# Kernel tuning notes

Measured on AMD Instinct MI355X. Metric: run time of the kernel, lower is better.

## Reference

```python
import jax, jax.numpy as jnp
import numpy as np

QLEN, MLEN, BSZ = 1024, 1024, 2
KLEN = QLEN + MLEN           # 2048, also rlen
D_MODEL, N_HEAD, D_HEAD = 1024, 16, 64
SCALE = 1.0 / (D_HEAD ** 0.5)
LN_EPS = 1e-5


def _rel_shift(x):
    # x: (qlen, klen, bsz, n_head). Torch-XL rel_shift via pad/reshape trick.
    q, k, b, n = x.shape
    zero_pad = jnp.zeros((q, 1, b, n), dtype=x.dtype)
    x_padded = jnp.concatenate([zero_pad, x], axis=1)   # (q, k+1, b, n)
    x_padded = x_padded.reshape(k + 1, q, b, n)[1:]      # drop first row
    return x_padded.reshape(q, k, b, n)


def _layer_norm(x, g, b):
    mu = jnp.mean(x, axis=-1, keepdims=True)
    var = jnp.mean(jnp.square(x - mu), axis=-1, keepdims=True)
    return (x - mu) * jax.lax.rsqrt(var + LN_EPS) * g + b


def setup_inputs() -> dict:
    key = jax.random.key(0)
    ks = jax.random.split(key, 9)
    w = jax.random.normal(ks[0], (QLEN, BSZ, D_MODEL), dtype=jnp.float32)
    r = jax.random.normal(ks[1], (KLEN, D_MODEL), dtype=jnp.float32)
    mems = jax.random.normal(ks[2], (MLEN, BSZ, D_MODEL), dtype=jnp.float32)
    # Causal mask with memory: query i may attend to key j <= i + MLEN.
    i = jnp.arange(QLEN)[:, None]
    j = jnp.arange(KLEN)[None, :]
    attn_mask = (j > i + MLEN)[:, :, None]  # (qlen, klen, 1) bool, dim==3 branch
    init = 0.02
    qkv_w = jax.random.normal(ks[3], (3 * N_HEAD * D_HEAD, D_MODEL), dtype=jnp.float32) * init
    r_w = jax.random.normal(ks[4], (N_HEAD * D_HEAD, D_MODEL), dtype=jnp.float32) * init
    o_w = jax.random.normal(ks[5], (D_MODEL, N_HEAD * D_HEAD), dtype=jnp.float32) * init
    ln_g = jnp.ones((D_MODEL,), dtype=jnp.float32)
    ln_b = jnp.zeros((D_MODEL,), dtype=jnp.float32)
    r_w_bias = jax.random.uniform(ks[6], (N_HEAD, D_HEAD), minval=-0.1, maxval=0.1, dtype=jnp.float32)
    r_r_bias = jax.random.uniform(ks[7], (N_HEAD, D_HEAD), minval=-0.1, maxval=0.1, dtype=jnp.float32)
    return {"w": w, "r": r, "mems": mems, "attn_mask": attn_mask,
            "qkv_w": qkv_w, "r_w": r_w, "o_w": o_w,
            "ln_g": ln_g, "ln_b": ln_b,
            "r_w_bias": r_w_bias, "r_r_bias": r_r_bias}


def reference(w, r, mems, attn_mask, qkv_w, r_w, o_w, ln_g, ln_b, r_w_bias, r_r_bias):
    qlen, bsz = w.shape[0], w.shape[1]
    cat = jnp.concatenate([mems, w], axis=0)                 # (klen, b, d_model)
    w_heads = cat @ qkv_w.T                                  # (klen, b, 3*n*d)
    w_head_q, w_head_k, w_head_v = jnp.split(w_heads, 3, axis=-1)
    klen = w_head_k.shape[0]
    w_head_q = w_head_q[-qlen:].reshape(qlen, bsz, N_HEAD, D_HEAD)
    w_head_k = w_head_k.reshape(klen, bsz, N_HEAD, D_HEAD)
    w_head_v = w_head_v.reshape(klen, bsz, N_HEAD, D_HEAD)
    r_head_k = (r @ r_w.T).reshape(r.shape[0], N_HEAD, D_HEAD)  # (rlen, n, d)

    AC = jnp.einsum('ibnd,jbnd->ijbn', w_head_q + r_w_bias, w_head_k)
    BD = _rel_shift(jnp.einsum('ibnd,jnd->ijbn', w_head_q + r_r_bias, r_head_k))
    attn_score = (AC + BD) * SCALE                           # (q, k, b, n)
    attn_score = jnp.where(attn_mask[:, :, :, None], -jnp.inf, attn_score)
    attn_prob = jax.nn.softmax(attn_score, axis=1)           # softmax over keys

    attn_vec = jnp.einsum('ijbn,jbnd->ibnd', attn_prob, w_head_v)
    attn_vec = attn_vec.reshape(qlen, bsz, N_HEAD * D_HEAD)
    attn_out = attn_vec @ o_w.T                              # (q, b, d_model)
    # post-LN residual (pre_lnorm=False)
    return _layer_norm(w + attn_out, ln_g, ln_b)
```

## Files before the change

### kernel.cpp

```cpp
#include <hip/hip_runtime.h>
#include <hip/hip_bf16.h>

#define QLEN 1024
#define MLEN 1024
#define KLEN 2048
#define BSZ 2
#define DMODEL 1024
#define NHEAD 16
#define DHEAD 64
#define SCALE_F 0.125f

typedef unsigned int u32;
typedef unsigned short u16;
typedef __attribute__((ext_vector_type(8))) short short8;
typedef __attribute__((ext_vector_type(4))) float f32x4;

__device__ __forceinline__ u16 f2bf(float f) {
  __hip_bfloat16 h = __float2bfloat16(f);
  return *reinterpret_cast<u16*>(&h);
}
__device__ __forceinline__ float bf2f(u16 u) {
  union { u32 w; float f; } c; c.w = ((u32)u) << 16; return c.f;
}
__device__ __forceinline__ float wave_sum(float v) {
#pragma unroll
  for (int o = 32; o > 0; o >>= 1) v += __shfl_xor(v, o);
  return v;
}

__global__ void detect_kernel(const void* __restrict__ lng, u32* __restrict__ flag) {
  if (threadIdx.x == 0 && blockIdx.x == 0) {
    u32 w = *(const u32*)lng;
    *flag = (w == 0x3F800000u) ? 0u : 1u;
  }
}

__global__ void conv_params(const void* __restrict__ lng, const void* __restrict__ lnb,
                            const void* __restrict__ rwb, const void* __restrict__ rrb,
                            float* __restrict__ PARAMS) {
  int i = blockIdx.x * 256 + threadIdx.x;
  u32 w0 = *(const u32*)lng;
  int f = (w0 != 0x3F800000u);
  int seg = i >> 10, off = i & 1023;
  const void* s = seg == 0 ? lng : seg == 1 ? lnb : seg == 2 ? rwb : rrb;
  PARAMS[i] = f ? bf2f(((const u16*)s)[off]) : ((const float*)s)[off];
}

__global__ void sentinel_kernel(u32* out) { out[threadIdx.x] = 0x49742400u;  }


#define GEMM_PREAMBLE()                                                        \
  __shared__ __align__(16) char lds2[2][128 * 128];                            \
  char* lA = lds2[0];                                                          \
  char* lB = lds2[1];                                                          \
  const int tid = threadIdx.x;                                                 \
  const int w_ = tid >> 6, l_ = tid & 63, lo = l_ & 15, g = l_ >> 4;           \
  const int wr = (w_ >> 1) * 64, wc = (w_ & 1) * 64;                           \
  f32x4 acc[4][4];                                                             \
  _Pragma("unroll") for (int mi = 0; mi < 4; ++mi)                             \
  _Pragma("unroll") for (int ni = 0; ni < 4; ++ni)                             \
      acc[mi][ni] = (f32x4){0.f, 0.f, 0.f, 0.f};

#define GEMM_MFMA_BODY()                                                       \
  _Pragma("unroll") for (int ks = 0; ks < 2; ++ks) {                           \
    short8 af[4], bf[4];                                                       \
    _Pragma("unroll") for (int mi = 0; mi < 4; ++mi) {                         \
      int r = wr + mi * 16 + lo;                                               \
      int c = ks * 4 + g;                                                      \
      af[mi] = *reinterpret_cast<const short8*>(lA + r * 128 + ((c ^ (r & 7)) * 16)); \
    }                                                                          \
    _Pragma("unroll") for (int ni = 0; ni < 4; ++ni) {                         \
      int r = wc + ni * 16 + lo;                                               \
      int c = ks * 4 + g;                                                      \
      bf[ni] = *reinterpret_cast<const short8*>(lB + r * 128 + ((c ^ (r & 7)) * 16)); \
    }                                                                          \
    _Pragma("unroll") for (int mi = 0; mi < 4; ++mi)                           \
    _Pragma("unroll") for (int ni = 0; ni < 4; ++ni)                           \
        acc[mi][ni] = __builtin_amdgcn_mfma_f32_16x16x32_bf16(af[mi], bf[ni], acc[mi][ni], 0, 0, 0); \
  }

__device__ __forceinline__ uint4 cvt8f32(const float* p) {
  float4 a = *reinterpret_cast<const float4*>(p);
  float4 b4 = *reinterpret_cast<const float4*>(p + 4);
  union { u16 us[8]; uint4 v; } o;
  o.us[0] = f2bf(a.x); o.us[1] = f2bf(a.y); o.us[2] = f2bf(a.z); o.us[3] = f2bf(a.w);
  o.us[4] = f2bf(b4.x); o.us[5] = f2bf(b4.y); o.us[6] = f2bf(b4.z); o.us[7] = f2bf(b4.w);
  return o.v;
}

__global__ __launch_bounds__(256) void gemm_qkv(
    const void* __restrict__ mems_raw, const void* __restrict__ w_raw,
    const void* __restrict__ qkvw_raw,
    const void* __restrict__ r_raw, const void* __restrict__ rw_raw,
    const float* __restrict__ PARAMS,
    u16* __restrict__ QWb, u16* __restrict__ QRb,
    u16* __restrict__ Kb, u16* __restrict__ VTb, u16* __restrict__ RKnb,
    const u32* __restrict__ flag) {
  const int col0 = blockIdx.x * 128;
  const int row0 = blockIdx.y * 128;
  const int f = (int)*flag;
  GEMM_PREAMBLE();

  if (col0 < 1024 && row0 < 2048) {
    for (int k0 = 0; k0 < DMODEL; k0 += 64) {
      __syncthreads();
      if (f) {
#pragma unroll
        for (int it = 0; it < 4; ++it) {
          int id = it * 256 + tid;
          int r = id >> 3, c = id & 7;
          uint4 va = *reinterpret_cast<const uint4*>((const u16*)r_raw + (size_t)(row0 + r) * DMODEL + k0 + c * 8);
          uint4 vb = *reinterpret_cast<const uint4*>((const u16*)rw_raw + (size_t)(col0 + r) * DMODEL + k0 + c * 8);
          *reinterpret_cast<uint4*>(lA + r * 128 + ((c ^ (r & 7)) * 16)) = va;
          *reinterpret_cast<uint4*>(lB + r * 128 + ((c ^ (r & 7)) * 16)) = vb;
        }
      } else {
#pragma unroll
        for (int it = 0; it < 4; ++it) {
          int id = it * 256 + tid;
          int r = id >> 3, c = id & 7;
          uint4 va = cvt8f32((const float*)r_raw + (size_t)(row0 + r) * DMODEL + k0 + c * 8);
          uint4 vb = cvt8f32((const float*)rw_raw + (size_t)(col0 + r) * DMODEL + k0 + c * 8);
          *reinterpret_cast<uint4*>(lA + r * 128 + ((c ^ (r & 7)) * 16)) = va;
          *reinterpret_cast<uint4*>(lB + r * 128 + ((c ^ (r & 7)) * 16)) = vb;
        }
      }
      __syncthreads();
      GEMM_MFMA_BODY();
    }
#pragma unroll
    for (int mi = 0; mi < 4; ++mi)
#pragma unroll
      for (int ni = 0; ni < 4; ++ni)
#pragma unroll
        for (int rr = 0; rr < 4; ++rr) {
          int t_ = row0 + wr + mi * 16 + g * 4 + rr;
          int col = col0 + wc + ni * 16 + lo;
          RKnb[((size_t)(col >> 6) * KLEN + t_) * 64 + (col & 63)] = f2bf(acc[mi][ni][rr]);
        }
    return;
  }

  for (int k0 = 0; k0 < DMODEL; k0 += 64) {
    __syncthreads();
    if (f) {
#pragma unroll
      for (int it = 0; it < 4; ++it) {
        int id = it * 256 + tid;
        int r = id >> 3, c = id & 7;
        int jb = row0 + r;
        const u16* asrc = jb < 2048 ? (const u16*)mems_raw + (size_t)jb * DMODEL
                                    : (const u16*)w_raw + (size_t)(jb - 2048) * DMODEL;
        uint4 va = *reinterpret_cast<const uint4*>(asrc + k0 + c * 8);
        uint4 vb = *reinterpret_cast<const uint4*>((const u16*)qkvw_raw + (size_t)(col0 + r) * DMODEL + k0 + c * 8);
        *reinterpret_cast<uint4*>(lA + r * 128 + ((c ^ (r & 7)) * 16)) = va;
        *reinterpret_cast<uint4*>(lB + r * 128 + ((c ^ (r & 7)) * 16)) = vb;
      }
    } else {
#pragma unroll
      for (int it = 0; it < 4; ++it) {
        int id = it * 256 + tid;
        int r = id >> 3, c = id & 7;
        int jb = row0 + r;
        const float* asrc = jb < 2048 ? (const float*)mems_raw + (size_t)jb * DMODEL
                                      : (const float*)w_raw + (size_t)(jb - 2048) * DMODEL;
        uint4 va = cvt8f32(asrc + k0 + c * 8);
        uint4 vb = cvt8f32((const float*)qkvw_raw + (size_t)(col0 + r) * DMODEL + k0 + c * 8);
        *reinterpret_cast<uint4*>(lA + r * 128 + ((c ^ (r & 7)) * 16)) = va;
        *reinterpret_cast<uint4*>(lB + r * 128 + ((c ^ (r & 7)) * 16)) = vb;
      }
    }
    __syncthreads();
    GEMM_MFMA_BODY();
  }

  const int which = col0 >> 10;
  if (which == 0) {
#pragma unroll
    for (int mi = 0; mi < 4; ++mi)
#pragma unroll
      for (int ni = 0; ni < 4; ++ni)
#pragma unroll
        for (int rr = 0; rr < 4; ++rr) {
          int row = row0 + wr + mi * 16 + g * 4 + rr;
          int col = col0 + wc + ni * 16 + lo;
          int i_ = (row >> 1) - 1024, b_ = row & 1;
          size_t ad = (((size_t)(b_ * 16 + (col >> 6))) * QLEN + i_) * 64 + (col & 63);
          float v = acc[mi][ni][rr];
          QWb[ad] = f2bf((v + PARAMS[2048 + col]) * SCALE_F);
          QRb[ad] = f2bf((v + PARAMS[3072 + col]) * SCALE_F);
        }
  } else if (which == 1) {
#pragma unroll
    for (int mi = 0; mi < 4; ++mi)
#pragma unroll
      for (int ni = 0; ni < 4; ++ni)
#pragma unroll
        for (int rr = 0; rr < 4; ++rr) {
          int row = row0 + wr + mi * 16 + g * 4 + rr;
          int col = col0 + wc + ni * 16 + lo;
          int j_ = row >> 1, b_ = row & 1;
          int cl = col - 1024;
          Kb[(((size_t)(b_ * 16 + (cl >> 6))) * KLEN + j_) * 64 + (cl & 63)] = f2bf(acc[mi][ni][rr]);
        }
  } else {
    __syncthreads();
    u16* ldsT = (u16*)lds2;
#pragma unroll
    for (int mi = 0; mi < 4; ++mi)
#pragma unroll
      for (int ni = 0; ni < 4; ++ni)
#pragma unroll
        for (int rr = 0; rr < 4; ++rr) {
          int rl = wr + mi * 16 + g * 4 + rr;
          int cl = wc + ni * 16 + lo;
          int rpp = (rl & 1) * 64 + (rl >> 1);
          ldsT[cl * 128 + (((rpp >> 3) ^ (cl & 7)) * 8) + (rpp & 7)] = f2bf(acc[mi][ni][rr]);
        }
    __syncthreads();
    int vc0 = col0 - 2048;
#pragma unroll
    for (int it = 0; it < 8; ++it) {
      int cid = it * 256 + tid;
      int c_l = cid >> 4;
      int j8 = cid & 15;
      uint4 vv = *reinterpret_cast<const uint4*>(ldsT + c_l * 128 + ((j8 ^ (c_l & 7)) * 8));
      int vcol = vc0 + c_l;
      int b_ = j8 >> 3;
      size_t dst = (((size_t)(b_ * 16 + (vcol >> 6))) * 64 + (vcol & 63)) * KLEN
                 + (row0 >> 1) + (j8 & 7) * 8;
      *reinterpret_cast<uint4*>(VTb + dst) = vv;
    }
  }
}

__global__ __launch_bounds__(256) void gemm_o(
    const u16* __restrict__ A, const void* __restrict__ ow_raw,
    float* __restrict__ C, const u32* __restrict__ flag) {
  const int col0 = blockIdx.x * 128;
  const int row0 = blockIdx.y * 128;
  const int f = (int)*flag;
  GEMM_PREAMBLE();
  for (int k0 = 0; k0 < DMODEL; k0 += 64) {
    __syncthreads();
    if (f) {
#pragma unroll
      for (int it = 0; it < 4; ++it) {
        int id = it * 256 + tid;
        int r = id >> 3, c = id & 7;
        uint4 va = *reinterpret_cast<const uint4*>(A + (size_t)(row0 + r) * DMODEL + k0 + c * 8);
        uint4 vb = *reinterpret_cast<const uint4*>((const u16*)ow_raw + (size_t)(col0 + r) * DMODEL + k0 + c * 8);
        *reinterpret_cast<uint4*>(lA + r * 128 + ((c ^ (r & 7)) * 16)) = va;
        *reinterpret_cast<uint4*>(lB + r * 128 + ((c ^ (r & 7)) * 16)) = vb;
      }
    } else {
#pragma unroll
      for (int it = 0; it < 4; ++it) {
        int id = it * 256 + tid;
        int r = id >> 3, c = id & 7;
        uint4 va = *reinterpret_cast<const uint4*>(A + (size_t)(row0 + r) * DMODEL + k0 + c * 8);
        uint4 vb = cvt8f32((const float*)ow_raw + (size_t)(col0 + r) * DMODEL + k0 + c * 8);
        *reinterpret_cast<uint4*>(lA + r * 128 + ((c ^ (r & 7)) * 16)) = va;
        *reinterpret_cast<uint4*>(lB + r * 128 + ((c ^ (r & 7)) * 16)) = vb;
      }
    }
    __syncthreads();
    GEMM_MFMA_BODY();
  }
#pragma unroll
  for (int mi = 0; mi < 4; ++mi)
#pragma unroll
    for (int ni = 0; ni < 4; ++ni)
#pragma unroll
      for (int rr = 0; rr < 4; ++rr) {
        int row = row0 + wr + mi * 16 + g * 4 + rr;
        int col = col0 + wc + ni * 16 + lo;
        C[(size_t)row * DMODEL + col] = acc[mi][ni][rr];
      }
}

__global__ __launch_bounds__(256) void attn_mfma(
    const u16* __restrict__ QWb, const u16* __restrict__ QRb,
    const u16* __restrict__ Kb, const u16* __restrict__ VTb,
    const u16* __restrict__ RKnb, float* __restrict__ PADO,
    float2* __restrict__ PML) {
  __shared__ __align__(16) char kt[8192];
  __shared__ __align__(16) char vt[8192];
  __shared__ __align__(16) char rt[2][8192];
  __shared__ __align__(16) char bfT[4 * 2560];
  __shared__ __align__(16) char pl[4 * 2048];

  const int tid = threadIdx.x;
  const int w = tid >> 6, l = tid & 63, lo = l & 15, g = l >> 4;
  const int gid = blockIdx.x;
  const int s = gid >> 9;
  const int r9 = gid & 511;
  const int lid = r9 & 255, hi = r9 >> 8;
  const int bn = lid & 31, q3 = lid >> 5;
  const int xi = hi ? (15 - q3) : q3;
  const int i0 = xi * 64;
  const int b = bn >> 4, n = bn & 15;
  const int nkt_full = xi + 17;
  const int h = (nkt_full + 1) >> 1;
  const int kst = s ? h : 0;
  const int kend = s ? nkt_full : h;

  const u16* qwp = QWb + (((size_t)bn * QLEN) + i0 + w * 16 + lo) * 64;
  const u16* qrp = QRb + (((size_t)bn * QLEN) + i0 + w * 16 + lo) * 64;
  short8 qw0 = *reinterpret_cast<const short8*>(qwp + g * 8);
  short8 qw1 = *reinterpret_cast<const short8*>(qwp + 32 + g * 8);
  short8 qr0 = *reinterpret_cast<const short8*>(qrp + g * 8);
  short8 qr1 = *reinterpret_cast<const short8*>(qrp + 32 + g * 8);

  const u16* kbp = Kb + (size_t)bn * KLEN * 64;
  const u16* vtp = VTb + (size_t)bn * 64 * KLEN;
  const u16* rp  = RKnb + (size_t)n * KLEN * 64;

  uint4 Rk[2], Rv[2], Rr[2];
  const int srow = tid >> 3, sc = tid & 7;
  const int j0p = kst * 64;

  {
    int m0 = kst + 15 - xi;
    char* rh = rt[m0 & 1];
#pragma unroll
    for (int it = 0; it < 2; ++it) {
      int row = srow + it * 32;
      int t = m0 * 64 + row;
      *reinterpret_cast<uint4*>(rh + row * 128 + ((sc ^ (row & 7)) * 16)) =
          *reinterpret_cast<const uint4*>(rp + (size_t)t * 64 + sc * 8);
    }
  }
#pragma unroll
  for (int it = 0; it < 2; ++it) {
    int row = srow + it * 32;
    Rk[it] = *reinterpret_cast<const uint4*>(kbp + (size_t)(j0p + row) * 64 + sc * 8);
    Rv[it] = *reinterpret_cast<const uint4*>(vtp + (size_t)row * KLEN + j0p + sc * 8);
    int t = (kst + 16 - xi) * 64 + row; t = t > KLEN - 1 ? KLEN - 1 : t;
    Rr[it] = *reinterpret_cast<const uint4*>(rp + (size_t)t * 64 + sc * 8);
  }

  f32x4 oacc[4];
  float m_r[4], lsum[4];
#pragma unroll
  for (int r = 0; r < 4; ++r) {
    oacc[r] = (f32x4){0.f, 0.f, 0.f, 0.f};
    m_r[r] = -1e30f; lsum[r] = 0.f;
  }

  for (int kti = kst; kti < kend; ++kti) {
    const int j0 = kti * 64;
    __syncthreads();
    {
      char* rh = rt[(kti + 16 - xi) & 1];
#pragma unroll
      for (int it = 0; it < 2; ++it) {
        int row = srow + it * 32;
        int sw = (sc ^ (row & 7)) * 16;
        *reinterpret_cast<uint4*>(kt + row * 128 + sw) = Rk[it];
        *reinterpret_cast<uint4*>(vt + row * 128 + sw) = Rv[it];
        *reinterpret_cast<uint4*>(rh + row * 128 + sw) = Rr[it];
      }
    }
    __syncthreads();
    if (kti + 1 < kend) {
      int j0n = j0 + 64;
      int mst = kti + 17 - xi;
#pragma unroll
      for (int it = 0; it < 2; ++it) {
        int row = srow + it * 32;
        Rk[it] = *reinterpret_cast<const uint4*>(kbp + (size_t)(j0n + row) * 64 + sc * 8);
        Rv[it] = *reinterpret_cast<const uint4*>(vtp + (size_t)row * KLEN + j0n + sc * 8);
        int t = mst * 64 + row; t = t > KLEN - 1 ? KLEN - 1 : t;
        Rr[it] = *reinterpret_cast<const uint4*>(rp + (size_t)t * 64 + sc * 8);
      }
    }
    const int hbase = (kti + 15 - xi) & 1;

    f32x4 ac[4];
    __builtin_amdgcn_s_setprio(1);
#pragma unroll
    for (int ct = 0; ct < 4; ++ct) {
      const char* kb = kt + (ct * 16 + lo) * 128;
      short8 k0 = *reinterpret_cast<const short8*>(kb + ((g ^ (lo & 7)) * 16));
      short8 k1 = *reinterpret_cast<const short8*>(kb + (((4 + g) ^ (lo & 7)) * 16));
      f32x4 a = {0.f, 0.f, 0.f, 0.f};
      a = __builtin_amdgcn_mfma_f32_16x16x32_bf16(qw0, k0, a, 0, 0, 0);
      a = __builtin_amdgcn_mfma_f32_16x16x32_bf16(qw1, k1, a, 0, 0, 0);
      ac[ct] = a;
    }
    __builtin_amdgcn_s_setprio(0);
    char* bfw = bfT + w * 2560;
    __builtin_amdgcn_s_setprio(1);
#pragma unroll
    for (int bb = 0; bb < 5; ++bb) {
      int bt = 3 - w + bb;
      int half = hbase ^ (bt >> 2);
      const char* rbase = rt[half] + ((bt & 3) * 16 + lo) * 128;
      short8 r0 = *reinterpret_cast<const short8*>(rbase + ((g ^ (lo & 7)) * 16));
      short8 r1 = *reinterpret_cast<const short8*>(rbase + (((4 + g) ^ (lo & 7)) * 16));
      f32x4 a = {0.f, 0.f, 0.f, 0.f};
      a = __builtin_amdgcn_mfma_f32_16x16x32_bf16(qr0, r0, a, 0, 0, 0);
      a = __builtin_amdgcn_mfma_f32_16x16x32_bf16(qr1, r1, a, 0, 0, 0);
      union { u16 us[4]; uint2 v2; } pk;
      pk.us[0] = f2bf(a[0]); pk.us[1] = f2bf(a[1]);
      pk.us[2] = f2bf(a[2]); pk.us[3] = f2bf(a[3]);
      int rel = bb * 16 + lo;
      int slot = ((((g >> 1) ^ (rel & 1)) * 2 + (g & 1)) ^ ((rel >> 2) & 3));
      *reinterpret_cast<uint2*>(bfw + rel * 32 + slot * 8) = pk.v2;
    }
    __builtin_amdgcn_s_setprio(0);
    const int relmax = i0 + MLEN - j0 + 15 + 16 * w;
    float rmax[4];
#pragma unroll
    for (int rr = 0; rr < 4; ++rr) rmax[rr] = -1e30f;
#pragma unroll
    for (int ct = 0; ct < 4; ++ct)
#pragma unroll
      for (int rr = 0; rr < 4; ++rr) {
        int rel = ct * 16 + lo - g * 4 - rr + 15;
        int slot = ((((g >> 1) ^ (rel & 1)) * 2 + (g & 1)) ^ ((rel >> 2) & 3));
        float bd = bf2f(*reinterpret_cast<const u16*>(bfw + rel * 32 + slot * 8 + rr * 2));
        float s2 = ac[ct][rr] + bd;
        s2 = rel > relmax ? -1e30f : s2;
        ac[ct][rr] = s2;
        rmax[rr] = fmaxf(rmax[rr], s2);
      }
    int upd = 0;
#pragma unroll
    for (int rr = 0; rr < 4; ++rr) {
      float rm = rmax[rr];
      rm = fmaxf(rm, __shfl_xor(rm, 1));
      rm = fmaxf(rm, __shfl_xor(rm, 2));
      rm = fmaxf(rm, __shfl_xor(rm, 4));
      rm = fmaxf(rm, __shfl_xor(rm, 8));
      rmax[rr] = rm;
      upd |= (rm > m_r[rr] + 8.0f);
    }
    if (__any(upd)) {
#pragma unroll
      for (int rr = 0; rr < 4; ++rr) {
        float mn = fmaxf(m_r[rr], rmax[rr]);
        float sc2 = __expf(m_r[rr] - mn);
        m_r[rr] = mn;
        lsum[rr] *= sc2;
#pragma unroll
        for (int dt = 0; dt < 4; ++dt) oacc[dt][rr] *= sc2;
      }
    }
#pragma unroll
    for (int ct = 0; ct < 4; ++ct)
#pragma unroll
      for (int rr = 0; rr < 4; ++rr) {
        float p = __expf(ac[ct][rr] - m_r[rr]);
        ac[ct][rr] = p;
        lsum[rr] += p;
      }
#pragma unroll
    for (int ct = 0; ct < 4; ++ct)
#pragma unroll
      for (int rr = 0; rr < 4; ++rr) {
        int rowp = g * 4 + rr;
        int col = ct * 16 + lo;
        int cblk = (col >> 3) ^ (rowp & 7);
        *reinterpret_cast<u16*>(pl + w * 2048 + rowp * 128 + cblk * 16 + (col & 7) * 2) = f2bf(ac[ct][rr]);
      }
    short8 pa0 = *reinterpret_cast<const short8*>(pl + w * 2048 + lo * 128 + ((g ^ (lo & 7)) * 16));
    short8 pa1 = *reinterpret_cast<const short8*>(pl + w * 2048 + lo * 128 + (((4 + g) ^ (lo & 7)) * 16));
    __builtin_amdgcn_s_setprio(1);
#pragma unroll
    for (int dt = 0; dt < 4; ++dt) {
      const char* vb = vt + (dt * 16 + lo) * 128;
      short8 v0 = *reinterpret_cast<const short8*>(vb + ((g ^ (lo & 7)) * 16));
      short8 v1 = *reinterpret_cast<const short8*>(vb + (((4 + g) ^ (lo & 7)) * 16));
      oacc[dt] = __builtin_amdgcn_mfma_f32_16x16x32_bf16(pa0, v0, oacc[dt], 0, 0, 0);
      oacc[dt] = __builtin_amdgcn_mfma_f32_16x16x32_bf16(pa1, v1, oacc[dt], 0, 0, 0);
    }
    __builtin_amdgcn_s_setprio(0);
  }

  float l_r[4];
#pragma unroll
  for (int rr = 0; rr < 4; ++rr) {
    float rs = lsum[rr];
    rs += __shfl_xor(rs, 1);
    rs += __shfl_xor(rs, 2);
    rs += __shfl_xor(rs, 4);
    rs += __shfl_xor(rs, 8);
    l_r[rr] = rs;
  }
#pragma unroll
  for (int rr = 0; rr < 4; ++rr) {
    int qi = i0 + w * 16 + g * 4 + rr;
    size_t rowg = ((size_t)(s * 32 + bn)) * QLEN + qi;
#pragma unroll
    for (int dt = 0; dt < 4; ++dt) {
      int d = dt * 16 + lo;
      PADO[rowg * 64 + d] = oacc[dt][rr];
    }
    if (lo == 0) {
      float2 ml; ml.x = m_r[rr]; ml.y = l_r[rr];
      PML[rowg] = ml;
    }
  }
}

__global__ __launch_bounds__(256) void combine_kernel(
    const float* __restrict__ PADO, const float2* __restrict__ PML,
    u16* __restrict__ AVb) {
  int idx = blockIdx.x * 256 + threadIdx.x;
  int row = idx >> 4;
  int c4 = (idx & 15) * 4;
  int bn = row >> 10, qi = row & 1023;
  int b = bn >> 4, n = bn & 15;
  float2 ml0 = PML[row];
  float2 ml1 = PML[32768 + row];
  float M = fmaxf(ml0.x, ml1.x);
  float e0 = __expf(ml0.x - M), e1 = __expf(ml1.x - M);
  float inv = 1.0f / (ml0.y * e0 + ml1.y * e1);
  f32x4 o0 = *reinterpret_cast<const f32x4*>(&PADO[(size_t)row * 64 + c4]);
  f32x4 o1 = *reinterpret_cast<const f32x4*>(&PADO[(size_t)(32768 + row) * 64 + c4]);
  union { u16 us[4]; uint2 v; } pk;
#pragma unroll
  for (int e = 0; e < 4; ++e)
    pk.us[e] = f2bf((o0[e] * e0 + o1[e] * e1) * inv);
  *reinterpret_cast<uint2*>(&AVb[((size_t)qi * BSZ + b) * DMODEL + n * 64 + c4]) = pk.v;
}

__global__ __launch_bounds__(256) void ln_kernel(const void* __restrict__ w_raw,
                                                 const float* __restrict__ AOUT,
                                                 const float* __restrict__ PARAMS,
                                                 void* __restrict__ out,
                                                 const u32* __restrict__ flag) {
  int row = blockIdx.x;
  int tid = threadIdx.x;
  __shared__ float buf[DMODEL];
  __shared__ float red[4];
  int f = (int)*flag;
  const float* ap = AOUT + (size_t)row * DMODEL;
  float lsum = 0.f;
  for (int c = tid; c < DMODEL; c += 256) {
    float wv = f ? bf2f(((const u16*)w_raw)[(size_t)row * DMODEL + c])
                 : ((const float*)w_raw)[(size_t)row * DMODEL + c];
    float v = wv + ap[c];
    buf[c] = v; lsum += v;
  }
  lsum = wave_sum(lsum);
  if ((tid & 63) == 0) red[tid >> 6] = lsum;
  __syncthreads();
  float mean = (red[0] + red[1] + red[2] + red[3]) * (1.0f / DMODEL);
  float lv = 0.f;
  for (int c = tid; c < DMODEL; c += 256) { float dv = buf[c] - mean; lv = fmaf(dv, dv, lv); }
  lv = wave_sum(lv);
  __syncthreads();
  if ((tid & 63) == 0) red[tid >> 6] = lv;
  __syncthreads();
  float rstd = rsqrtf((red[0] + red[1] + red[2] + red[3]) * (1.0f / DMODEL) + 1e-5f);
  for (int c = tid; c < DMODEL; c += 256) {
    float o = (buf[c] - mean) * rstd * PARAMS[c] + PARAMS[1024 + c];
    if (f) ((__hip_bfloat16*)out)[(size_t)row * DMODEL + c] = __float2bfloat16(o);
    else   ((float*)out)[(size_t)row * DMODEL + c] = o;
  }
}

extern "C" void kernel_launch(void* const* d_in, const int* in_sizes, int n_in,
                              void* d_out, int out_size, void* d_ws, size_t ws_size,
                              hipStream_t stream) {
  const void* w_in    = d_in[0];
  const void* r_in    = d_in[1];
  const void* mems_in = d_in[2];
  const void* qkvw_in = d_in[4];
  const void* rw_in   = d_in[5];
  const void* ow_in   = d_in[6];
  const void* lng_in  = d_in[7];
  const void* lnb_in  = d_in[8];
  const void* rwb_in  = d_in[9];
  const void* rrb_in  = d_in[10];

  char* ws = (char*)d_ws;
  u32* flag = (u32*)ws;
  char* cur = ws + 256;
  auto alloc = [&](size_t bytes) { char* p = cur; cur += (bytes + 255) & ~(size_t)255; return p; };

  float* PARAMS = (float*)alloc(4096 * 4);
  u16* QWb  = (u16*)alloc((size_t)BSZ * NHEAD * QLEN * 64 * 2);
  u16* QRb  = (u16*)alloc((size_t)BSZ * NHEAD * QLEN * 64 * 2);
  u16* Kb   = (u16*)alloc((size_t)BSZ * NHEAD * KLEN * 64 * 2);
  u16* VTb  = (u16*)alloc((size_t)BSZ * NHEAD * 64 * KLEN * 2);
  u16* RKnb = (u16*)alloc((size_t)NHEAD * KLEN * 64 * 2);
  u16* AVb  = (u16*)alloc((size_t)QLEN * BSZ * DMODEL * 2);
  float* AOUT = (float*)alloc((size_t)QLEN * BSZ * DMODEL * 4);
  float* PADO = (float*)alloc((size_t)2 * 32 * QLEN * 64 * 4);
  float2* PML = (float2*)alloc((size_t)2 * 32 * QLEN * 8);
  size_t need = (size_t)(cur - ws);

  if (ws_size < need || out_size != QLEN * BSZ * DMODEL || n_in < 11) {
    sentinel_kernel<<<1, 256, 0, stream>>>((u32*)d_out);
    return;
  }

  detect_kernel<<<1, 64, 0, stream>>>(lng_in, flag);
  conv_params<<<16, 256, 0, stream>>>(lng_in, lnb_in, rwb_in, rrb_in, PARAMS);

  dim3 b256(256);
  gemm_qkv<<<dim3(24, 32), b256, 0, stream>>>(mems_in, w_in, qkvw_in, r_in, rw_in,
                                              PARAMS, QWb, QRb, Kb, VTb, RKnb, flag);
  attn_mfma<<<1024, b256, 0, stream>>>(QWb, QRb, Kb, VTb, RKnb, PADO, PML);
  combine_kernel<<<2048, b256, 0, stream>>>(PADO, PML, AVb);
  gemm_o<<<dim3(8, 16), b256, 0, stream>>>(AVb, ow_in, AOUT, flag);
  ln_kernel<<<QLEN * BSZ, b256, 0, stream>>>(w_in, AOUT, PARAMS, d_out, flag);
}
```

Before: 218.1 us.

## Drop split-K attention and combine kernel; normalize and write output directly

The attention kernel no longer splits each query tile's key range across two blocks. Each block now walks the full key range and writes the normalized bf16 output directly, so the combine kernel and its fp32 partial buffers go away. The P-staging LDS buffer is merged into the bias scratch buffer to cut shared memory, and launch bounds request 3 blocks per CU. This saves a kernel launch and the partial-result traffic, but halves the grid to 512 blocks with longer, unevenly sized per-block loops, which may underfill 256 CUs.

```diff
diff --git a/kernel.cpp b/kernel.cpp
--- a/kernel.cpp
+++ b/kernel.cpp
@@ -279,31 +279,24 @@
       }
 }
 
-__global__ __launch_bounds__(256) void attn_mfma(
+__global__ __launch_bounds__(256, 3) void attn_mfma(
     const u16* __restrict__ QWb, const u16* __restrict__ QRb,
     const u16* __restrict__ Kb, const u16* __restrict__ VTb,
-    const u16* __restrict__ RKnb, float* __restrict__ PADO,
-    float2* __restrict__ PML) {
+    const u16* __restrict__ RKnb, u16* __restrict__ AVb) {
   __shared__ __align__(16) char kt[8192];
   __shared__ __align__(16) char vt[8192];
   __shared__ __align__(16) char rt[2][8192];
-  __shared__ __align__(16) char bfT[4 * 2560];
-  __shared__ __align__(16) char pl[4 * 2048];
+  __shared__ __align__(16) char scratch[4 * 2560];
 
   const int tid = threadIdx.x;
   const int w = tid >> 6, l = tid & 63, lo = l & 15, g = l >> 4;
   const int gid = blockIdx.x;
-  const int s = gid >> 9;
-  const int r9 = gid & 511;
-  const int lid = r9 & 255, hi = r9 >> 8;
+  const int lid = gid & 255, hi = gid >> 8;
   const int bn = lid & 31, q3 = lid >> 5;
   const int xi = hi ? (15 - q3) : q3;
   const int i0 = xi * 64;
   const int b = bn >> 4, n = bn & 15;
-  const int nkt_full = xi + 17;
-  const int h = (nkt_full + 1) >> 1;
-  const int kst = s ? h : 0;
-  const int kend = s ? nkt_full : h;
+  const int nkt = xi + 17;
 
   const u16* qwp = QWb + (((size_t)bn * QLEN) + i0 + w * 16 + lo) * 64;
   const u16* qrp = QRb + (((size_t)bn * QLEN) + i0 + w * 16 + lo) * 64;
@@ -318,10 +311,9 @@
 
   uint4 Rk[2], Rv[2], Rr[2];
   const int srow = tid >> 3, sc = tid & 7;
-  const int j0p = kst * 64;
 
   {
-    int m0 = kst + 15 - xi;
+    int m0 = 15 - xi;
     char* rh = rt[m0 & 1];
 #pragma unroll
     for (int it = 0; it < 2; ++it) {
@@ -334,9 +326,9 @@
 #pragma unroll
   for (int it = 0; it < 2; ++it) {
     int row = srow + it * 32;
-    Rk[it] = *reinterpret_cast<const uint4*>(kbp + (size_t)(j0p + row) * 64 + sc * 8);
-    Rv[it] = *reinterpret_cast<const uint4*>(vtp + (size_t)row * KLEN + j0p + sc * 8);
-    int t = (kst + 16 - xi) * 64 + row; t = t > KLEN - 1 ? KLEN - 1 : t;
+    Rk[it] = *reinterpret_cast<const uint4*>(kbp + (size_t)row * 64 + sc * 8);
+    Rv[it] = *reinterpret_cast<const uint4*>(vtp + (size_t)row * KLEN + sc * 8);
+    int t = (16 - xi) * 64 + row; t = t > KLEN - 1 ? KLEN - 1 : t;
     Rr[it] = *reinterpret_cast<const uint4*>(rp + (size_t)t * 64 + sc * 8);
   }
 
@@ -348,7 +340,7 @@
     m_r[r] = -1e30f; lsum[r] = 0.f;
   }
 
-  for (int kti = kst; kti < kend; ++kti) {
+  for (int kti = 0; kti < nkt; ++kti) {
     const int j0 = kti * 64;
     __syncthreads();
     {
@@ -363,7 +355,7 @@
       }
     }
     __syncthreads();
-    if (kti + 1 < kend) {
+    if (kti + 1 < nkt) {
       int j0n = j0 + 64;
       int mst = kti + 17 - xi;
 #pragma unroll
@@ -390,7 +382,7 @@
       ac[ct] = a;
     }
     __builtin_amdgcn_s_setprio(0);
-    char* bfw = bfT + w * 2560;
+    char* bfw = scratch + w * 2560;
     __builtin_amdgcn_s_setprio(1);
 #pragma unroll
     for (int bb = 0; bb < 5; ++bb) {
@@ -463,10 +455,10 @@
         int rowp = g * 4 + rr;
         int col = ct * 16 + lo;
         int cblk = (col >> 3) ^ (rowp & 7);
-        *reinterpret_cast<u16*>(pl + w * 2048 + rowp * 128 + cblk * 16 + (col & 7) * 2) = f2bf(ac[ct][rr]);
-      }
-    short8 pa0 = *reinterpret_cast<const short8*>(pl + w * 2048 + lo * 128 + ((g ^ (lo & 7)) * 16));
-    short8 pa1 = *reinterpret_cast<const short8*>(pl + w * 2048 + lo * 128 + (((4 + g) ^ (lo & 7)) * 16));
+        *reinterpret_cast<u16*>(bfw + rowp * 128 + cblk * 16 + (col & 7) * 2) = f2bf(ac[ct][rr]);
+      }
+    short8 pa0 = *reinterpret_cast<const short8*>(bfw + lo * 128 + ((g ^ (lo & 7)) * 16));
+    short8 pa1 = *reinterpret_cast<const short8*>(bfw + lo * 128 + (((4 + g) ^ (lo & 7)) * 16));
     __builtin_amdgcn_s_setprio(1);
 #pragma unroll
     for (int dt = 0; dt < 4; ++dt) {
@@ -479,7 +471,6 @@
     __builtin_amdgcn_s_setprio(0);
   }
 
-  float l_r[4];
 #pragma unroll
   for (int rr = 0; rr < 4; ++rr) {
     float rs = lsum[rr];
@@ -487,44 +478,14 @@
     rs += __shfl_xor(rs, 2);
     rs += __shfl_xor(rs, 4);
     rs += __shfl_xor(rs, 8);
-    l_r[rr] = rs;
-  }
-#pragma unroll
-  for (int rr = 0; rr < 4; ++rr) {
+    float inv = 1.0f / rs;
     int qi = i0 + w * 16 + g * 4 + rr;
-    size_t rowg = ((size_t)(s * 32 + bn)) * QLEN + qi;
 #pragma unroll
     for (int dt = 0; dt < 4; ++dt) {
       int d = dt * 16 + lo;
-      PADO[rowg * 64 + d] = oacc[dt][rr];
-    }
-    if (lo == 0) {
-      float2 ml; ml.x = m_r[rr]; ml.y = l_r[rr];
-      PML[rowg] = ml;
-    }
-  }
-}
-
-__global__ __launch_bounds__(256) void combine_kernel(
-    const float* __restrict__ PADO, const float2* __restrict__ PML,
-    u16* __restrict__ AVb) {
-  int idx = blockIdx.x * 256 + threadIdx.x;
-  int row = idx >> 4;
-  int c4 = (idx & 15) * 4;
-  int bn = row >> 10, qi = row & 1023;
-  int b = bn >> 4, n = bn & 15;
-  float2 ml0 = PML[row];
-  float2 ml1 = PML[32768 + row];
-  float M = fmaxf(ml0.x, ml1.x);
-  float e0 = __expf(ml0.x - M), e1 = __expf(ml1.x - M);
-  float inv = 1.0f / (ml0.y * e0 + ml1.y * e1);
-  f32x4 o0 = *reinterpret_cast<const f32x4*>(&PADO[(size_t)row * 64 + c4]);
-  f32x4 o1 = *reinterpret_cast<const f32x4*>(&PADO[(size_t)(32768 + row) * 64 + c4]);
-  union { u16 us[4]; uint2 v; } pk;
-#pragma unroll
-  for (int e = 0; e < 4; ++e)
-    pk.us[e] = f2bf((o0[e] * e0 + o1[e] * e1) * inv);
-  *reinterpret_cast<uint2*>(&AVb[((size_t)qi * BSZ + b) * DMODEL + n * 64 + c4]) = pk.v;
+      AVb[((size_t)qi * BSZ + b) * DMODEL + n * 64 + d] = f2bf(oacc[dt][rr] * inv);
+    }
+  }
 }
 
 __global__ __launch_bounds__(256) void ln_kernel(const void* __restrict__ w_raw,
@@ -590,8 +551,6 @@
   u16* RKnb = (u16*)alloc((size_t)NHEAD * KLEN * 64 * 2);
   u16* AVb  = (u16*)alloc((size_t)QLEN * BSZ * DMODEL * 2);
   float* AOUT = (float*)alloc((size_t)QLEN * BSZ * DMODEL * 4);
-  float* PADO = (float*)alloc((size_t)2 * 32 * QLEN * 64 * 4);
-  float2* PML = (float2*)alloc((size_t)2 * 32 * QLEN * 8);
   size_t need = (size_t)(cur - ws);
 
   if (ws_size < need || out_size != QLEN * BSZ * DMODEL || n_in < 11) {
@@ -605,8 +564,7 @@
   dim3 b256(256);
   gemm_qkv<<<dim3(24, 32), b256, 0, stream>>>(mems_in, w_in, qkvw_in, r_in, rw_in,
                                               PARAMS, QWb, QRb, Kb, VTb, RKnb, flag);
-  attn_mfma<<<1024, b256, 0, stream>>>(QWb, QRb, Kb, VTb, RKnb, PADO, PML);
-  combine_kernel<<<2048, b256, 0, stream>>>(PADO, PML, AVb);
+  attn_mfma<<<512, b256, 0, stream>>>(QWb, QRb, Kb, VTb, RKnb, AVb);
   gemm_o<<<dim3(8, 16), b256, 0, stream>>>(AVb, ow_in, AOUT, flag);
   ln_kernel<<<QLEN * BSZ, b256, 0, stream>>>(w_in, AOUT, PARAMS, d_out, flag);
 }
```

Measured after the change: 251.1 us. +15.1%, slower.
